# Kernel optimization log

Measured on AMD Instinct MI355X. Metric: run time of the kernel, lower is better.

The kernel has to match this reference:

```python
import jax, jax.numpy as jnp
import numpy as np

B, T, K, H = 2, 4096, 512, 8


def setup_inputs() -> dict:
    key = jax.random.key(0)
    ks = jax.random.split(key, 6)
    scale = 1.0 / np.sqrt(K)
    return {
        "x": jax.random.normal(ks[0], (B, T, K), dtype=jnp.float32),
        "padding_mask": jnp.ones((B, T), dtype=jnp.int32),
        "Wq": jax.random.normal(ks[1], (K, K), dtype=jnp.float32) * scale,
        "Wk": jax.random.normal(ks[2], (K, K), dtype=jnp.float32) * scale,
        "Wv": jax.random.normal(ks[3], (K, K), dtype=jnp.float32) * scale,
        "Wu": jax.random.normal(ks[4], (K, K), dtype=jnp.float32) * scale,
        "bu": jnp.zeros((K,), dtype=jnp.float32),
    }


def reference(x, padding_mask, Wq, Wk, Wv, Wu, bu):
    b, t, e = x.shape
    h = H
    s = e // h
    # torch Linear: y = x @ W.T
    q = (x @ Wq.T).reshape(b, t, h, s).transpose(0, 2, 1, 3)  # (b,h,t,s)
    k = (x @ Wk.T).reshape(b, t, h, s).transpose(0, 2, 1, 3)
    v = (x @ Wv.T).reshape(b, t, h, s).transpose(0, 2, 1, 3)
    inv4 = e ** (-0.25)
    q = q * inv4
    k = k * inv4
    dot = jnp.einsum("bhqs,bhks->bhqk", q, k)  # (b,h,t,t)
    neg_inf = jnp.float32(-jnp.inf)
    # causal mask (self.mask == True)
    causal = jnp.triu(jnp.ones((t, t), dtype=bool), k=1)
    dot = jnp.where(causal[None, None], neg_inf, dot)
    # padding mask applied along the QUERY dimension, as in the original
    dot = jnp.where(padding_mask[:, None, :, None] == 0, neg_inf, dot)
    attn = jax.nn.softmax(dot, axis=-1)
    out = jnp.einsum("bhqk,bhks->bhqs", attn, v)  # (b,h,t,s)
    out = out.transpose(0, 2, 1, 3).reshape(b, t, e)
    return out @ Wu.T + bu
```

## Files before the change

### kernel.cpp

```cpp
#include <hip/hip_runtime.h>
#include <hip/hip_bf16.h>

#define BB 2
#define TT 4096
#define KK 512
#define HH 8
#define SS 64
#define MM 8192

typedef __attribute__((ext_vector_type(8))) short bf16x8;
typedef __attribute__((ext_vector_type(4))) float f32x4;
typedef unsigned int u32;
typedef __attribute__((ext_vector_type(2))) u32 u32x2;
typedef __attribute__((ext_vector_type(4))) u32 u32x4;

#define SCL_QK 0.25250488f

static __device__ __forceinline__ short f2b(float f) {
    union { float f; unsigned u; } v;
    v.f = f;
    unsigned r = v.u + 0x7fffu + ((v.u >> 16) & 1u);
    return (short)(r >> 16);
}

static __device__ __forceinline__ u32 cvt2(float lo, float hi) {
    u32 r;
    asm("v_cvt_pk_bf16_f32 %0, %1, %2" : "=v"(r) : "v"(lo), "v"(hi));
    return r;
}

static __device__ __forceinline__ void stage_cvt(short* lds, const float* __restrict__ src, int tid) {
    int row = tid >> 1, c0 = (tid & 1) * 32;
    const float4* g = (const float4*)(src + (size_t)row * KK + c0);
    u32* d = (u32*)(lds + row * 72 + c0);
#pragma unroll
    for (int i = 0; i < 4; ++i) {
        float4 a = g[2 * i], b = g[2 * i + 1];
        u32x4 w = { cvt2(a.x, a.y), cvt2(a.z, a.w), cvt2(b.x, b.y), cvt2(b.z, b.w) };
        *(u32x4*)(d + 4 * i) = w;
    }
}

static __device__ __forceinline__ void stage_b16(short* lds, const short* __restrict__ src, int tid) {
    int row = tid >> 1, c0 = (tid & 1) * 32;
    const bf16x8* g = (const bf16x8*)(src + (size_t)row * KK + c0);
    bf16x8 v0 = g[0], v1 = g[1], v2 = g[2], v3 = g[3];
    short* d = lds + row * 72 + c0;
    *(bf16x8*)(d)      = v0;
    *(bf16x8*)(d + 8)  = v1;
    *(bf16x8*)(d + 16) = v2;
    *(bf16x8*)(d + 24) = v3;
}

__global__ __launch_bounds__(256) void proj_qkv(
    const float* __restrict__ x,
    const float* __restrict__ Wq, const float* __restrict__ Wk, const float* __restrict__ Wv,
    short* __restrict__ q, short* __restrict__ k, short* __restrict__ v)
{
    __shared__ short aS[128 * 72];
    __shared__ short bS[128 * 72];
    int nt = blockIdx.x, mt = blockIdx.y, z = blockIdx.z;
    const float* W = (z == 0) ? Wq : ((z == 1) ? Wk : Wv);
    short* dst = (z == 0) ? q : ((z == 1) ? k : v);
    int tid = threadIdx.x, wave = tid >> 6, lane = tid & 63;
    int lr = lane & 15, lg = lane >> 4;
    int wr = wave >> 1, wc = wave & 1;

    f32x4 acc[4][4];
#pragma unroll
    for (int m = 0; m < 4; ++m)
#pragma unroll
        for (int n = 0; n < 4; ++n) acc[m][n] = (f32x4){0.f, 0.f, 0.f, 0.f};

    for (int k0 = 0; k0 < KK; k0 += 64) {
        __syncthreads();
        stage_cvt(aS, x + (size_t)(mt * 128) * KK + k0, tid);
        stage_cvt(bS, W + (size_t)(nt * 128) * KK + k0, tid);
        __syncthreads();
#pragma unroll
        for (int kc = 0; kc < 2; ++kc) {
            bf16x8 af[4], bw[4];
#pragma unroll
            for (int m = 0; m < 4; ++m)
                af[m] = *(const bf16x8*)&aS[(wr * 64 + m * 16 + lr) * 72 + kc * 32 + lg * 8];
#pragma unroll
            for (int n = 0; n < 4; ++n)
                bw[n] = *(const bf16x8*)&bS[(wc * 64 + n * 16 + lr) * 72 + kc * 32 + lg * 8];
#pragma unroll
            for (int m = 0; m < 4; ++m)
#pragma unroll
                for (int n = 0; n < 4; ++n)
                    acc[m][n] = __builtin_amdgcn_mfma_f32_16x16x32_bf16(af[m], bw[n], acc[m][n], 0, 0, 0);
        }
    }

#pragma unroll
    for (int n = 0; n < 4; ++n) {
        int nn = nt * 128 + wc * 64 + n * 16 + lr;
        int h = nn >> 6, s = nn & 63;
#pragma unroll
        for (int m = 0; m < 4; ++m) {
            int m0 = mt * 128 + wr * 64 + m * 16 + lg * 4;
            int b = m0 >> 12, t0 = m0 & (TT - 1);
            if (z == 2) {
                u32x2 pk = { cvt2(acc[m][n][0], acc[m][n][1]), cvt2(acc[m][n][2], acc[m][n][3]) };
                *(u32x2*)&dst[(((size_t)(b * HH + h)) * SS + s) * TT + t0] = pk;
            } else {
#pragma unroll
                for (int r = 0; r < 4; ++r)
                    dst[(((size_t)(b * HH + h)) * TT + (t0 + r)) * SS + s] = f2b(acc[m][n][r] * SCL_QK);
            }
        }
    }
}

__global__ __launch_bounds__(256) void proj_out(
    const short* __restrict__ a, const float* __restrict__ Wu,
    const float* __restrict__ bu, float* __restrict__ out)
{
    __shared__ short aS[128 * 72];
    __shared__ short bS[128 * 72];
    int nt = blockIdx.x, mt = blockIdx.y;
    int tid = threadIdx.x, wave = tid >> 6, lane = tid & 63;
    int lr = lane & 15, lg = lane >> 4;
    int wr = wave >> 1, wc = wave & 1;

    f32x4 acc[4][4];
#pragma unroll
    for (int m = 0; m < 4; ++m)
#pragma unroll
        for (int n = 0; n < 4; ++n) acc[m][n] = (f32x4){0.f, 0.f, 0.f, 0.f};

    for (int k0 = 0; k0 < KK; k0 += 64) {
        __syncthreads();
        stage_b16(aS, a + (size_t)(mt * 128) * KK + k0, tid);
        stage_cvt(bS, Wu + (size_t)(nt * 128) * KK + k0, tid);
        __syncthreads();
#pragma unroll
        for (int kc = 0; kc < 2; ++kc) {
            bf16x8 af[4], bw[4];
#pragma unroll
            for (int m = 0; m < 4; ++m)
                af[m] = *(const bf16x8*)&aS[(wr * 64 + m * 16 + lr) * 72 + kc * 32 + lg * 8];
#pragma unroll
            for (int n = 0; n < 4; ++n)
                bw[n] = *(const bf16x8*)&bS[(wc * 64 + n * 16 + lr) * 72 + kc * 32 + lg * 8];
#pragma unroll
            for (int m = 0; m < 4; ++m)
#pragma unroll
                for (int n = 0; n < 4; ++n)
                    acc[m][n] = __builtin_amdgcn_mfma_f32_16x16x32_bf16(af[m], bw[n], acc[m][n], 0, 0, 0);
        }
    }

#pragma unroll
    for (int n = 0; n < 4; ++n) {
        int nn = nt * 128 + wc * 64 + n * 16 + lr;
        float bias = bu[nn];
#pragma unroll
        for (int m = 0; m < 4; ++m) {
            int mm = mt * 128 + wr * 64 + m * 16 + lg * 4;
#pragma unroll
            for (int r = 0; r < 4; ++r)
                out[(size_t)(mm + r) * KK + nn] = acc[m][n][r] + bias;
        }
    }
}

__global__ __launch_bounds__(256) void flash_attn(
    const short* __restrict__ Q, const short* __restrict__ Kv,
    const short* __restrict__ Vt, short* __restrict__ Oout)
{
    __shared__ short k_lds[64][72];
    __shared__ short v_lds[64][72];
    __shared__ short p_lds[4][16][72];

    int u = blockIdx.x;
    int i = u & 15, bh = (u >> 4) & 15, j = u >> 8;
    int sl = j * 16 + i;
    int qt = (sl < 16) ? (63 - sl) : (sl < 32 ? (sl - 16) : (sl < 48 ? (79 - sl) : (sl - 32)));

    int tid = threadIdx.x, wave = tid >> 6, lane = tid & 63;
    int lr = lane & 15, lg = lane >> 4;
    int b = bh >> 3, h = bh & 7;

    const short* Qb = Q + (size_t)bh * TT * SS;
    const short* Kb = Kv + (size_t)bh * TT * SS;
    const short* Vb = Vt + (size_t)bh * SS * TT;

    int urow = tid >> 3, useg = tid & 7;

    int qrow0 = qt * 64 + wave * 16;

    bf16x8 a_q[2];
#pragma unroll
    for (int kc = 0; kc < 2; ++kc)
        a_q[kc] = *(const bf16x8*)&Qb[(size_t)(qrow0 + lr) * SS + kc * 32 + lg * 8];

    f32x4 o[4];
#pragma unroll
    for (int n = 0; n < 4; ++n) o[n] = (f32x4){0.f, 0.f, 0.f, 0.f};
    float m_run = -INFINITY, l_run = 0.f;

    int nkv = qt + 1;
    bf16x8 kr0, kr1, vr0, vr1;
    kr0 = *(const bf16x8*)&Kb[(size_t)urow * SS + useg * 8];
    kr1 = *(const bf16x8*)&Kb[(size_t)(urow + 32) * SS + useg * 8];
    vr0 = *(const bf16x8*)&Vb[(size_t)urow * TT + useg * 8];
    vr1 = *(const bf16x8*)&Vb[(size_t)(urow + 32) * TT + useg * 8];

    for (int kt = 0; kt < nkv; ++kt) {
        __syncthreads();
        *(bf16x8*)&k_lds[urow][useg * 8]      = kr0;
        *(bf16x8*)&k_lds[urow + 32][useg * 8] = kr1;
        *(bf16x8*)&v_lds[urow][useg * 8]      = vr0;
        *(bf16x8*)&v_lds[urow + 32][useg * 8] = vr1;
        if (kt + 1 < nkv) {
            int kn = kt + 1;
            kr0 = *(const bf16x8*)&Kb[(size_t)(kn * 64 + urow) * SS + useg * 8];
            kr1 = *(const bf16x8*)&Kb[(size_t)(kn * 64 + urow + 32) * SS + useg * 8];
            vr0 = *(const bf16x8*)&Vb[(size_t)urow * TT + kn * 64 + useg * 8];
            vr1 = *(const bf16x8*)&Vb[(size_t)(urow + 32) * TT + kn * 64 + useg * 8];
        }
        __syncthreads();

        f32x4 sc[4];
#pragma unroll
        for (int ct = 0; ct < 4; ++ct) sc[ct] = (f32x4){0.f, 0.f, 0.f, 0.f};
        __builtin_amdgcn_s_setprio(1);
#pragma unroll
        for (int kc = 0; kc < 2; ++kc) {
#pragma unroll
            for (int ct = 0; ct < 4; ++ct) {
                bf16x8 kf = *(const bf16x8*)&k_lds[ct * 16 + lr][kc * 32 + lg * 8];
                sc[ct] = __builtin_amdgcn_mfma_f32_16x16x32_bf16(kf, a_q[kc], sc[ct], 0, 0, 0);
            }
        }
        __builtin_amdgcn_s_setprio(0);
        if (kt == qt) {
#pragma unroll
            for (int ct = 0; ct < 4; ++ct) {
                int kv0 = kt * 64 + ct * 16 + lg * 4;
                int qq = qrow0 + lr;
#pragma unroll
                for (int r = 0; r < 4; ++r)
                    if (kv0 + r > qq) sc[ct][r] = -INFINITY;
            }
        }
        float mx = -INFINITY;
#pragma unroll
        for (int ct = 0; ct < 4; ++ct)
#pragma unroll
            for (int r = 0; r < 4; ++r) mx = fmaxf(mx, sc[ct][r]);
        mx = fmaxf(mx, __shfl_xor(mx, 16));
        mx = fmaxf(mx, __shfl_xor(mx, 32));
        if (!__all(mx <= m_run + 8.0f)) {
            float mnew = fmaxf(m_run, mx);
            float corr = __builtin_amdgcn_exp2f(m_run - mnew);
            l_run *= corr;
#pragma unroll
            for (int st = 0; st < 4; ++st)
#pragma unroll
                for (int r = 0; r < 4; ++r) o[st][r] *= corr;
            m_run = mnew;
        }
        float s0 = 0.f;
#pragma unroll
        for (int ct = 0; ct < 4; ++ct)
#pragma unroll
            for (int r = 0; r < 4; ++r) {
                float pf = __builtin_amdgcn_exp2f(sc[ct][r] - m_run);
                sc[ct][r] = pf;
                s0 += pf;
            }
        s0 += __shfl_xor(s0, 16);
        s0 += __shfl_xor(s0, 32);
        l_run += s0;

#pragma unroll
        for (int ct = 0; ct < 4; ++ct) {
            u32x2 pk = { cvt2(sc[ct][0], sc[ct][1]), cvt2(sc[ct][2], sc[ct][3]) };
            *(u32x2*)&p_lds[wave][lr][ct * 16 + lg * 4] = pk;
        }
        asm volatile("s_waitcnt lgkmcnt(0)" ::: "memory");
        __builtin_amdgcn_s_setprio(1);
#pragma unroll
        for (int kc = 0; kc < 2; ++kc) {
            bf16x8 pb = *(const bf16x8*)&p_lds[wave][lr][kc * 32 + lg * 8];
#pragma unroll
            for (int st = 0; st < 4; ++st) {
                bf16x8 vf = *(const bf16x8*)&v_lds[st * 16 + lr][kc * 32 + lg * 8];
                o[st] = __builtin_amdgcn_mfma_f32_16x16x32_bf16(vf, pb, o[st], 0, 0, 0);
            }
        }
        __builtin_amdgcn_s_setprio(0);
    }

    float inv = 1.f / l_run;
    int t = qrow0 + lr;
#pragma unroll
    for (int st = 0; st < 4; ++st) {
        u32x2 ov = { cvt2(o[st][0] * inv, o[st][1] * inv), cvt2(o[st][2] * inv, o[st][3] * inv) };
        *(u32x2*)&Oout[(size_t)(b * TT + t) * KK + h * 64 + st * 16 + lg * 4] = ov;
    }
}

extern "C" void kernel_launch(void* const* d_in, const int* in_sizes, int n_in,
                              void* d_out, int out_size, void* d_ws, size_t ws_size,
                              hipStream_t stream) {
    const float* x  = (const float*)d_in[0];
    const float* Wq = (const float*)d_in[2];
    const float* Wk = (const float*)d_in[3];
    const float* Wv = (const float*)d_in[4];
    const float* Wu = (const float*)d_in[5];
    const float* bu = (const float*)d_in[6];
    float* out = (float*)d_out;

    short* q_ws = (short*)d_ws;
    short* k_ws = q_ws + (size_t)MM * KK;
    short* v_ws = k_ws + (size_t)MM * KK;
    short* a_ws = v_ws + (size_t)MM * KK;

    dim3 gQKV(KK / 128, MM / 128, 3);
    proj_qkv<<<gQKV, 256, 0, stream>>>(x, Wq, Wk, Wv, q_ws, k_ws, v_ws);

    flash_attn<<<1024, 256, 0, stream>>>(q_ws, k_ws, v_ws, a_ws);

    dim3 gO(KK / 128, MM / 128);
    proj_out<<<gO, 256, 0, stream>>>(a_ws, Wu, bu, out);
}
```

Baseline: 232.3 us.

## Pre-convert inputs to bf16 and stage GEMM tiles via global_load_lds

Adds a separate kernel that converts x and all four weight matrices to bf16 once, reusing the attention output workspace for x. Both projection GEMMs then stage tiles straight from global memory into LDS with global_load_lds instead of loading fp32 and converting in registers. The LDS row padding is dropped, which may cause bank conflicts. The output projection moves to 64-row tiles to launch more blocks. The cost is an extra launch plus a full fp32-read/bf16-write pass over x, traded against the repeated per-tile conversion of x and the weights inside the GEMMs.

New measurement: 200.8 us. 1.16x faster.

```diff
diff --git a/kernel.cpp b/kernel.cpp
--- a/kernel.cpp
+++ b/kernel.cpp
@@ -29,42 +29,54 @@
     return r;
 }
 
-static __device__ __forceinline__ void stage_cvt(short* lds, const float* __restrict__ src, int tid) {
-    int row = tid >> 1, c0 = (tid & 1) * 32;
-    const float4* g = (const float4*)(src + (size_t)row * KK + c0);
-    u32* d = (u32*)(lds + row * 72 + c0);
-#pragma unroll
-    for (int i = 0; i < 4; ++i) {
-        float4 a = g[2 * i], b = g[2 * i + 1];
-        u32x4 w = { cvt2(a.x, a.y), cvt2(a.z, a.w), cvt2(b.x, b.y), cvt2(b.z, b.w) };
-        *(u32x4*)(d + 4 * i) = w;
-    }
-}
-
-static __device__ __forceinline__ void stage_b16(short* lds, const short* __restrict__ src, int tid) {
-    int row = tid >> 1, c0 = (tid & 1) * 32;
-    const bf16x8* g = (const bf16x8*)(src + (size_t)row * KK + c0);
-    bf16x8 v0 = g[0], v1 = g[1], v2 = g[2], v3 = g[3];
-    short* d = lds + row * 72 + c0;
-    *(bf16x8*)(d)      = v0;
-    *(bf16x8*)(d + 8)  = v1;
-    *(bf16x8*)(d + 16) = v2;
-    *(bf16x8*)(d + 24) = v3;
+#define GLOAD16(g, l) __builtin_amdgcn_global_load_lds( \
+    (const __attribute__((address_space(1))) void*)(g), \
+    (__attribute__((address_space(3))) void*)(l), 16, 0, 0)
+
+__global__ __launch_bounds__(256) void cvt_bf16(
+    const float* __restrict__ x,
+    const float* __restrict__ Wq, const float* __restrict__ Wk,
+    const float* __restrict__ Wv, const float* __restrict__ Wu,
+    short* __restrict__ xb, short* __restrict__ wb)
+{
+    const int NX = MM * KK;
+    const int NW = KK * KK;
+    int idx = blockIdx.x * blockDim.x + threadIdx.x;
+    int total = (NX + 4 * NW) >> 3;
+    for (int g = idx; g < total; g += gridDim.x * blockDim.x) {
+        int e = g << 3;
+        const float* src; short* dst;
+        if (e < NX) { src = x + e; dst = xb + e; }
+        else {
+            int gg = e - NX;
+            int wsel = gg >> 18;
+            int off = gg & (NW - 1);
+            src = (wsel == 0 ? Wq : wsel == 1 ? Wk : wsel == 2 ? Wv : Wu) + off;
+            dst = wb + gg;
+        }
+        float4 a = *(const float4*)src;
+        float4 b = *(const float4*)(src + 4);
+        u32x4 wv = { cvt2(a.x, a.y), cvt2(a.z, a.w), cvt2(b.x, b.y), cvt2(b.z, b.w) };
+        *(u32x4*)dst = wv;
+    }
 }
 
 __global__ __launch_bounds__(256) void proj_qkv(
-    const float* __restrict__ x,
-    const float* __restrict__ Wq, const float* __restrict__ Wk, const float* __restrict__ Wv,
+    const short* __restrict__ xb, const short* __restrict__ wb,
     short* __restrict__ q, short* __restrict__ k, short* __restrict__ v)
 {
-    __shared__ short aS[128 * 72];
-    __shared__ short bS[128 * 72];
+    __shared__ short aS[128 * 64];
+    __shared__ short bS[128 * 64];
     int nt = blockIdx.x, mt = blockIdx.y, z = blockIdx.z;
-    const float* W = (z == 0) ? Wq : ((z == 1) ? Wk : Wv);
+    const short* W = wb + (size_t)z * KK * KK;
     short* dst = (z == 0) ? q : ((z == 1) ? k : v);
     int tid = threadIdx.x, wave = tid >> 6, lane = tid & 63;
     int lr = lane & 15, lg = lane >> 4;
     int wr = wave >> 1, wc = wave & 1;
+    int l8 = lane >> 3, c8 = lane & 7;
+
+    const short* Ag = xb + (size_t)(mt * 128) * KK;
+    const short* Bg = W + (size_t)(nt * 128) * KK;
 
     f32x4 acc[4][4];
 #pragma unroll
@@ -74,18 +86,22 @@
 
     for (int k0 = 0; k0 < KK; k0 += 64) {
         __syncthreads();
-        stage_cvt(aS, x + (size_t)(mt * 128) * KK + k0, tid);
-        stage_cvt(bS, W + (size_t)(nt * 128) * KK + k0, tid);
+#pragma unroll
+        for (int i = 0; i < 4; ++i) {
+            int row = wave * 32 + i * 8 + l8;
+            GLOAD16(Ag + (size_t)row * KK + k0 + c8 * 8, &aS[(wave * 32 + i * 8) * 64]);
+            GLOAD16(Bg + (size_t)row * KK + k0 + c8 * 8, &bS[(wave * 32 + i * 8) * 64]);
+        }
         __syncthreads();
 #pragma unroll
         for (int kc = 0; kc < 2; ++kc) {
             bf16x8 af[4], bw[4];
 #pragma unroll
             for (int m = 0; m < 4; ++m)
-                af[m] = *(const bf16x8*)&aS[(wr * 64 + m * 16 + lr) * 72 + kc * 32 + lg * 8];
+                af[m] = *(const bf16x8*)&aS[(wr * 64 + m * 16 + lr) * 64 + kc * 32 + lg * 8];
 #pragma unroll
             for (int n = 0; n < 4; ++n)
-                bw[n] = *(const bf16x8*)&bS[(wc * 64 + n * 16 + lr) * 72 + kc * 32 + lg * 8];
+                bw[n] = *(const bf16x8*)&bS[(wc * 64 + n * 16 + lr) * 64 + kc * 32 + lg * 8];
 #pragma unroll
             for (int m = 0; m < 4; ++m)
 #pragma unroll
@@ -115,38 +131,50 @@
 }
 
 __global__ __launch_bounds__(256) void proj_out(
-    const short* __restrict__ a, const float* __restrict__ Wu,
+    const short* __restrict__ a, const short* __restrict__ Wub,
     const float* __restrict__ bu, float* __restrict__ out)
 {
-    __shared__ short aS[128 * 72];
-    __shared__ short bS[128 * 72];
+    __shared__ short aS[64 * 64];
+    __shared__ short bS[128 * 64];
     int nt = blockIdx.x, mt = blockIdx.y;
     int tid = threadIdx.x, wave = tid >> 6, lane = tid & 63;
     int lr = lane & 15, lg = lane >> 4;
     int wr = wave >> 1, wc = wave & 1;
-
-    f32x4 acc[4][4];
-#pragma unroll
-    for (int m = 0; m < 4; ++m)
+    int l8 = lane >> 3, c8 = lane & 7;
+
+    const short* Ag = a + (size_t)(mt * 64) * KK;
+    const short* Bg = Wub + (size_t)(nt * 128) * KK;
+
+    f32x4 acc[2][4];
+#pragma unroll
+    for (int m = 0; m < 2; ++m)
 #pragma unroll
         for (int n = 0; n < 4; ++n) acc[m][n] = (f32x4){0.f, 0.f, 0.f, 0.f};
 
     for (int k0 = 0; k0 < KK; k0 += 64) {
         __syncthreads();
-        stage_b16(aS, a + (size_t)(mt * 128) * KK + k0, tid);
-        stage_cvt(bS, Wu + (size_t)(nt * 128) * KK + k0, tid);
+#pragma unroll
+        for (int i = 0; i < 2; ++i) {
+            int row = wave * 16 + i * 8 + l8;
+            GLOAD16(Ag + (size_t)row * KK + k0 + c8 * 8, &aS[(wave * 16 + i * 8) * 64]);
+        }
+#pragma unroll
+        for (int i = 0; i < 4; ++i) {
+            int row = wave * 32 + i * 8 + l8;
+            GLOAD16(Bg + (size_t)row * KK + k0 + c8 * 8, &bS[(wave * 32 + i * 8) * 64]);
+        }
         __syncthreads();
 #pragma unroll
         for (int kc = 0; kc < 2; ++kc) {
-            bf16x8 af[4], bw[4];
-#pragma unroll
-            for (int m = 0; m < 4; ++m)
-                af[m] = *(const bf16x8*)&aS[(wr * 64 + m * 16 + lr) * 72 + kc * 32 + lg * 8];
+            bf16x8 af[2], bw[4];
+#pragma unroll
+            for (int m = 0; m < 2; ++m)
+                af[m] = *(const bf16x8*)&aS[(wr * 32 + m * 16 + lr) * 64 + kc * 32 + lg * 8];
 #pragma unroll
             for (int n = 0; n < 4; ++n)
-                bw[n] = *(const bf16x8*)&bS[(wc * 64 + n * 16 + lr) * 72 + kc * 32 + lg * 8];
-#pragma unroll
-            for (int m = 0; m < 4; ++m)
+                bw[n] = *(const bf16x8*)&bS[(wc * 64 + n * 16 + lr) * 64 + kc * 32 + lg * 8];
+#pragma unroll
+            for (int m = 0; m < 2; ++m)
 #pragma unroll
                 for (int n = 0; n < 4; ++n)
                     acc[m][n] = __builtin_amdgcn_mfma_f32_16x16x32_bf16(af[m], bw[n], acc[m][n], 0, 0, 0);
@@ -158,8 +186,8 @@
         int nn = nt * 128 + wc * 64 + n * 16 + lr;
         float bias = bu[nn];
 #pragma unroll
-        for (int m = 0; m < 4; ++m) {
-            int mm = mt * 128 + wr * 64 + m * 16 + lg * 4;
+        for (int m = 0; m < 2; ++m) {
+            int mm = mt * 64 + wr * 32 + m * 16 + lg * 4;
 #pragma unroll
             for (int r = 0; r < 4; ++r)
                 out[(size_t)(mm + r) * KK + nn] = acc[m][n][r] + bias;
@@ -316,16 +344,19 @@
     const float* bu = (const float*)d_in[6];
     float* out = (float*)d_out;
 
-    short* q_ws = (short*)d_ws;
-    short* k_ws = q_ws + (size_t)MM * KK;
-    short* v_ws = k_ws + (size_t)MM * KK;
-    short* a_ws = v_ws + (size_t)MM * KK;
+    short* q_ws  = (short*)d_ws;
+    short* k_ws  = q_ws + (size_t)MM * KK;
+    short* v_ws  = k_ws + (size_t)MM * KK;
+    short* a_ws  = v_ws + (size_t)MM * KK;
+    short* wb_ws = a_ws + (size_t)MM * KK;
+
+    cvt_bf16<<<2560, 256, 0, stream>>>(x, Wq, Wk, Wv, Wu, a_ws, wb_ws);
 
     dim3 gQKV(KK / 128, MM / 128, 3);
-    proj_qkv<<<gQKV, 256, 0, stream>>>(x, Wq, Wk, Wv, q_ws, k_ws, v_ws);
+    proj_qkv<<<gQKV, 256, 0, stream>>>(a_ws, wb_ws, q_ws, k_ws, v_ws);
 
     flash_attn<<<1024, 256, 0, stream>>>(q_ws, k_ws, v_ws, a_ws);
 
-    dim3 gO(KK / 128, MM / 128);
-    proj_out<<<gO, 256, 0, stream>>>(a_ws, Wu, bu, out);
-}
+    dim3 gO(KK / 128, MM / 64);
+    proj_out<<<gO, 256, 0, stream>>>(a_ws, wb_ws + 3 * (size_t)KK * KK, bu, out);
+}
```
